# Kernel optimization log

Measured on AMD Instinct MI355X. Metric: run time of the kernel, lower is better.

## Reference

```python
import jax, jax.numpy as jnp
import numpy as np

N, E, D, H, L, R = 10000, 48000, 768, 4, 4, 3
NEG = -1e30


def setup_inputs() -> dict:
    key = jax.random.key(0)
    ks = jax.random.split(key, 16)
    s = 0.02
    return {
        'node_features': jax.random.normal(ks[0], (N, D), jnp.float32),
        'edge_index': jax.random.randint(ks[1], (2, E), 0, N, jnp.int64 if jax.config.jax_enable_x64 else jnp.int32),
        'edge_type': jax.random.randint(ks[2], (E,), 0, R, jnp.int64 if jax.config.jax_enable_x64 else jnp.int32),
        'rel_W': jax.random.normal(ks[3], (R, D, D), jnp.float32) * s,
        'rel_b': jnp.zeros((R, D), jnp.float32),
        'gat_W': jax.random.normal(ks[4], (L, D, H * D), jnp.float32) * s,
        'gat_att_src': jax.random.normal(ks[5], (L, H, D), jnp.float32) * s,
        'gat_att_dst': jax.random.normal(ks[6], (L, H, D), jnp.float32) * s,
        'gat_bias': jnp.zeros((L, D), jnp.float32),
        'proj_W1': jax.random.normal(ks[7], (D, 512), jnp.float32) * s,
        'proj_b1': jnp.zeros((512,), jnp.float32),
        'proj_W2': jax.random.normal(ks[8], (512, D), jnp.float32) * s,
        'proj_b2': jnp.zeros((D,), jnp.float32),
    }


def _gat_rel(g, a_src, a_dst, bias, src, dst, emask):
    # g: [N,H,D] transformed per-head node features; PyG GATConv with
    # add_self_loops=True, leaky_relu slope 0.2, concat=False (head mean).
    alpha_s = jnp.einsum('nhd,hd->nh', g, a_src)   # [N,H]
    alpha_d = jnp.einsum('nhd,hd->nh', g, a_dst)   # [N,H]
    e = jax.nn.leaky_relu(alpha_s[src] + alpha_d[dst], 0.2)  # [E,H]
    e = jnp.where(emask[:, None], e, NEG)          # mask other relations
    e_self = jax.nn.leaky_relu(alpha_s + alpha_d, 0.2)       # [N,H] self loops
    m = jax.ops.segment_max(e, dst, num_segments=N)
    m = jnp.maximum(m, e_self)                     # stable softmax max per dst
    p = jnp.where(emask[:, None], jnp.exp(e - m[dst]), 0.0)  # [E,H]
    p_self = jnp.exp(e_self - m)                   # [N,H]
    denom = jax.ops.segment_sum(p, dst, num_segments=N) + p_self
    msg = jax.ops.segment_sum(p[:, :, None] * g[src], dst, num_segments=N)
    msg = msg + p_self[:, :, None] * g             # [N,H,D]
    out = msg / denom[:, :, None]
    return out.mean(axis=1) + bias                 # concat=False -> head mean


def reference(node_features, edge_index, edge_type, rel_W, rel_b, gat_W,
              gat_att_src, gat_att_dst, gat_bias, proj_W1, proj_b1,
              proj_W2, proj_b2):
    src, dst = edge_index[0], edge_index[1]
    h = node_features
    for l in range(L):
        h_new = jnp.zeros_like(h)
        for r in range(R):
            emask = edge_type == r
            t = h @ rel_W[r] + rel_b[r]                    # relation transform
            g = (t @ gat_W[l]).reshape(N, H, D)            # [N,H,D]
            h_new = h_new + _gat_rel(g, gat_att_src[l], gat_att_dst[l],
                                     gat_bias[l], src, dst, emask)
        h = jax.nn.relu(h + h_new)                         # residual + relu
    positions = jax.nn.relu(h @ proj_W1 + proj_b1) @ proj_W2 + proj_b2
    return positions, h
```

## Files before the change

kernel.cpp:

```cpp
#include <hip/hip_runtime.h>
#include <stdint.h>

#define NN 10000
#define NE 48000
#define DIM 768
#define NH 4
#define NL 4
#define NR 3
#define HD 3072
#define NPAD 10240
#define NRD (NR*DIM)
#define SCN (NR*NN)
#define SCB ((SCN+255)/256)

typedef __attribute__((ext_vector_type(8))) short bf16x8;
typedef __attribute__((ext_vector_type(4))) float f32x4;

__device__ __forceinline__ unsigned short f2b(float f){
  union {float f; unsigned u;} v; v.f=f;
  unsigned r = v.u + 0x7FFFu + ((v.u>>16)&1u);
  return (unsigned short)(r>>16);
}
__device__ __forceinline__ float b2f(unsigned short b){
  union {unsigned u; float f;} v; v.u = ((unsigned)b)<<16; return v.f;
}

__device__ __forceinline__ void gl_lds16(const void* g, void* l){
  __builtin_amdgcn_global_load_lds(
    reinterpret_cast<const __attribute__((address_space(1))) uint32_t*>(reinterpret_cast<uintptr_t>(g)),
    reinterpret_cast<__attribute__((address_space(3))) uint32_t*>(reinterpret_cast<uintptr_t>(l)),
    16, 0, 0);
}

#define MPH(P) \
  { _Pragma("unroll") for (int ni=0; ni<NB; ni++) \
      _Pragma("unroll") for (int ks=0; ks<2; ks++) \
        acc[P][ni] = __builtin_amdgcn_mfma_f32_16x16x32_bf16( \
          a[P][ks], b[ni][ks], acc[P][ni],0,0,0); }

template<int MODE>
__global__ __launch_bounds__(512, 4)
void gemmU(const unsigned short* __restrict__ A, const unsigned short* __restrict__ Bt,
           void* __restrict__ C, unsigned short* __restrict__ C2,
           const float* __restrict__ RH, const float* __restrict__ bias, float bscale,
           int K, int Mvalid, int ldc)
{
  constexpr int NB     = 2;
  constexpr int ABYTES = 16384;
  constexpr int SLOT   = 32768;
  __shared__ char lds2[2*SLOT];

  const int tid = threadIdx.x;
  const int lane = tid & 63;
  const int wv = tid >> 6;
  const int wr = wv >> 2;
  const int wc = wv & 3;
  const int fr = lane & 15;
  const int fs = lane >> 4;

  int bx, by;
  {
    int fid = blockIdx.y * gridDim.x + blockIdx.x;
    if ((gridDim.y & 7) == 0){
      int xcd = fid & 7, slot = fid >> 3;
      bx = slot % gridDim.x;
      by = (slot / gridDim.x) * 8 + xcd;
    } else { bx = blockIdx.x; by = blockIdx.y; }
  }

  const unsigned short* Ag = A + (size_t)by * 128 * K;
  const unsigned short* Bg = Bt + (size_t)bx * 128 * K;
  const int T = K >> 6;

  f32x4 acc[4][NB];
  #pragma unroll
  for (int i=0;i<4;i++)
    #pragma unroll
    for (int j=0;j<NB;j++) acc[i][j] = (f32x4){0.f,0.f,0.f,0.f};

  auto stage = [&](int t2, int c){
    char* region = lds2 + (t2 & 1) * SLOT;
    const unsigned short* G = Ag;
    int off = c * 8192 + tid * 16;
    if (c >= 2){ G = Bg; off -= ABYTES; region += ABYTES; }
    int row = off >> 7;
    int srcslot = ((off >> 4) & 7) ^ (row & 7);
    gl_lds16((const char*)(G + (size_t)row * K + (size_t)t2 * 64) + (srcslot << 4),
             region + off);
  };

  #pragma unroll
  for (int c=0;c<4;c++) stage(0,c);
  __builtin_amdgcn_sched_barrier(0);
  stage(1,0); stage(1,1);
  __builtin_amdgcn_sched_barrier(0);

  for (int t=0; t<T; ++t){
    const char* As_ = lds2 + (t&1)*SLOT;
    const char* Bs_ = As_ + ABYTES;

    if (t < T-1) asm volatile("s_waitcnt vmcnt(2)" ::: "memory");
    else         asm volatile("s_waitcnt vmcnt(0)" ::: "memory");
    __builtin_amdgcn_s_barrier();

    bf16x8 a[4][2], b[NB][2];
    #pragma unroll
    for (int ni=0; ni<NB; ni++){
      const int row = wc*32 + ni*16 + fr;
      #pragma unroll
      for (int ks=0; ks<2; ks++){
        const int bo = row*128 + ((((ks<<2)+fs) ^ (row&7))<<4);
        b[ni][ks] = *(const bf16x8*)(Bs_ + bo);
      }
    }
    #pragma unroll
    for (int mi=0; mi<2; mi++){
      const int row = wr*64 + mi*16 + fr;
      #pragma unroll
      for (int ks=0; ks<2; ks++){
        const int bo = row*128 + ((((ks<<2)+fs) ^ (row&7))<<4);
        a[mi][ks] = *(const bf16x8*)(As_ + bo);
      }
    }
    if (t+1 < T) stage(t+1, 2);
    asm volatile("s_waitcnt lgkmcnt(0)" ::: "memory");
    __builtin_amdgcn_sched_barrier(0);
    __builtin_amdgcn_s_setprio(1); MPH(0); __builtin_amdgcn_s_setprio(0);
    __builtin_amdgcn_s_barrier();

    #pragma unroll
    for (int mi=2; mi<4; mi++){
      const int row = wr*64 + mi*16 + fr;
      #pragma unroll
      for (int ks=0; ks<2; ks++){
        const int bo = row*128 + ((((ks<<2)+fs) ^ (row&7))<<4);
        a[mi][ks] = *(const bf16x8*)(As_ + bo);
      }
    }
    if (t+1 < T) stage(t+1, 3);
    asm volatile("s_waitcnt lgkmcnt(0)" ::: "memory");
    __builtin_amdgcn_sched_barrier(0);
    __builtin_amdgcn_s_setprio(1); MPH(1); __builtin_amdgcn_s_setprio(0);
    __builtin_amdgcn_s_barrier();

    if (t+2 < T) stage(t+2, 0);
    __builtin_amdgcn_s_setprio(1); MPH(2); __builtin_amdgcn_s_setprio(0);
    __builtin_amdgcn_s_barrier();

    if (t+2 < T) stage(t+2, 1);
    __builtin_amdgcn_s_setprio(1); MPH(3); __builtin_amdgcn_s_setprio(0);
  }

  const int cr = (lane>>4)<<2, cc = lane&15;
  #pragma unroll
  for (int mi=0; mi<4; mi++){
    #pragma unroll
    for (int ni=0; ni<NB; ni++){
      const int col = bx*128 + wc*32 + ni*16 + cc;
      const float bv = bias ? bscale*bias[col] : 0.0f;
      #pragma unroll
      for (int j=0; j<4; j++){
        const int row = by*128 + wr*64 + mi*16 + cr + j;
        if (row < Mvalid){
          const size_t o = (size_t)row*ldc + col;
          float v = acc[mi][ni][j] + bv;
          if (MODE==2) v = v>0.f?v:0.f;
          if (MODE==0)      ((float*)C)[o] = v;
          else if (MODE==1 || MODE==2) ((unsigned short*)C)[o] = f2b(v);
          else {
            float w = RH[o] + v;
            w = w>0.f?w:0.f;
            ((float*)C)[o] = w; C2[o] = f2b(w);
          }
        }
      }
    }
  }
}

__global__ void k_init(const float* __restrict__ nf, float* __restrict__ h, unsigned short* __restrict__ hb){
  for (size_t i = (size_t)blockIdx.x*256+threadIdx.x; i < (size_t)NPAD*DIM; i += (size_t)gridDim.x*256){
    float v = (i < (size_t)NN*DIM) ? nf[i] : 0.0f;
    h[i]=v; hb[i]=f2b(v);
  }
}
__global__ void k_transpose(const float* __restrict__ in, unsigned short* __restrict__ out,
                            int rows, int cols, long in_bs, long out_bs){
  __shared__ float tile[32][33];
  int b = blockIdx.z;
  int r0 = blockIdx.y*32, c0 = blockIdx.x*32;
  int tx = threadIdx.x & 31, ty = threadIdx.x >> 5;
  const float* ip = in + (size_t)b*in_bs;
  unsigned short* op = out + (size_t)b*out_bs;
  #pragma unroll
  for (int i=ty;i<32;i+=8) tile[i][tx] = ip[(size_t)(r0+i)*cols + c0+tx];
  __syncthreads();
  #pragma unroll
  for (int i=ty;i<32;i+=8) op[(size_t)(c0+i)*rows + r0+tx] = f2b(tile[tx][i]);
}
__global__ void k_gatws(const float* __restrict__ gat_W, unsigned short* __restrict__ out){
  __shared__ float tile[32][33];
  int z = blockIdx.z; int l = z>>2, h = z&3;
  size_t base = (size_t)l*DIM*HD + (size_t)h*DIM;
  int r0 = blockIdx.y*32, c0 = blockIdx.x*32;
  int tx = threadIdx.x & 31, ty = threadIdx.x >> 5;
  #pragma unroll
  for (int i=ty;i<32;i+=8) tile[i][tx] = gat_W[base + (size_t)(r0+i)*HD + c0+tx];
  __syncthreads();
  #pragma unroll
  for (int i=ty;i<32;i+=8) out[base + (size_t)(c0+i)*HD + r0+tx] = f2b(0.25f*tile[tx][i]);
}

__global__ __launch_bounds__(256) void k_vsrc(const float* __restrict__ gat_W, const float* __restrict__ a_src,
                       const float* __restrict__ a_dst, float* __restrict__ vs, float* __restrict__ vd){
  int gw = blockIdx.x*4 + (threadIdx.x>>6);
  if (gw >= NL*DIM) return;
  int l = gw/DIM;
  int lane = threadIdx.x & 63;
  const float* grow = gat_W + (size_t)gw*HD;
  #pragma unroll
  for (int h=0;h<NH;h++){
    const float* asr = a_src + ((size_t)l*NH + h)*DIM;
    const float* adr = a_dst + ((size_t)l*NH + h)*DIM;
    float s=0.f,d=0.f;
    for (int dd=lane; dd<DIM; dd+=64){
      float gv = grow[h*DIM+dd];
      s += gv*asr[dd]; d += gv*adr[dd];
    }
    #pragma unroll
    for (int o=32;o>=1;o>>=1){ s += __shfl_xor(s,o,64); d += __shfl_xor(d,o,64); }
    if (lane==0){ vs[(size_t)gw*NH+h]=s; vd[(size_t)gw*NH+h]=d; }
  }
}
__global__ __launch_bounds__(256) void k_wa(const float* __restrict__ rel_W, const float* __restrict__ vs,
                     const float* __restrict__ vd, float* __restrict__ was, float* __restrict__ wad){
  int gw = blockIdx.x*4 + (threadIdx.x>>6);
  if (gw >= NL*NR*DIM) return;
  int lr = gw/DIM, k = gw%DIM;
  int l = lr/NR, r = lr%NR;
  int lane = threadIdx.x & 63;
  const float* wrow = rel_W + ((size_t)r*DIM + k)*DIM;
  float s0=0,s1=0,s2=0,s3=0,d0=0,d1=0,d2=0,d3=0;
  for (int q=lane; q<DIM; q+=64){
    float w = wrow[q];
    const float4 v1 = *(const float4*)(vs + ((size_t)l*DIM+q)*NH);
    const float4 v2 = *(const float4*)(vd + ((size_t)l*DIM+q)*NH);
    s0+=w*v1.x; s1+=w*v1.y; s2+=w*v1.z; s3+=w*v1.w;
    d0+=w*v2.x; d1+=w*v2.y; d2+=w*v2.z; d3+=w*v2.w;
  }
  #pragma unroll
  for (int o=32;o>=1;o>>=1){
    s0+=__shfl_xor(s0,o,64); s1+=__shfl_xor(s1,o,64); s2+=__shfl_xor(s2,o,64); s3+=__shfl_xor(s3,o,64);
    d0+=__shfl_xor(d0,o,64); d1+=__shfl_xor(d1,o,64); d2+=__shfl_xor(d2,o,64); d3+=__shfl_xor(d3,o,64);
  }
  if (lane==0){
    float4* ps = (float4*)(was + (size_t)gw*NH); *ps = make_float4(s0,s1,s2,s3);
    float4* pd = (float4*)(wad + (size_t)gw*NH); *pd = make_float4(d0,d1,d2,d3);
  }
}
__global__ void k_bsd(const float* __restrict__ rel_b, const float* __restrict__ vs, const float* __restrict__ vd,
                      float* __restrict__ bs, float* __restrict__ bd){
  int t = threadIdx.x; if (t >= NL*NR*NH) return;
  int l = t/(NR*NH), r = (t/NH)%NR, h = t%NH;
  float s=0.f,d=0.f;
  for (int q=0;q<DIM;q++){
    float b = rel_b[r*DIM+q];
    s += b*vs[((size_t)l*DIM+q)*NH+h];
    d += b*vd[((size_t)l*DIM+q)*NH+h];
  }
  bs[t]=s; bd[t]=d;
}

__global__ void k_count(const int* __restrict__ et, const int* __restrict__ ei, int* __restrict__ counts){
  int e = blockIdx.x*256+threadIdx.x; if (e>=NE) return;
  atomicAdd(&counts[et[e]*NN + ei[NE+e]], 1);
}
__global__ void k_scan1(const int* __restrict__ counts, int* __restrict__ excl, int* __restrict__ part){
  __shared__ int tmp[256];
  int b = blockIdx.x, t = threadIdx.x, idx = b*256+t;
  int v = (idx<SCN)? counts[idx] : 0;
  tmp[t]=v; __syncthreads();
  #pragma unroll
  for (int off=1; off<256; off<<=1){
    int x = (t>=off)? tmp[t-off] : 0;
    __syncthreads(); tmp[t]+=x; __syncthreads();
  }
  if (idx<SCN) excl[idx] = tmp[t]-v;
  if (t==255) part[b] = tmp[255];
}
__global__ void k_scan2(int* __restrict__ part){
  if (threadIdx.x==0){
    int c=0;
    for (int i=0;i<SCB;i++){ int v=part[i]; part[i]=c; c+=v; }
    part[SCB]=c;
  }
}
__global__ void k_scan3(int* __restrict__ rs, const int* __restrict__ part, int* __restrict__ cursor){
  int b = blockIdx.x, idx = b*256+threadIdx.x;
  if (idx<SCN){
    int e = rs[idx] + part[b];
    rs[idx]=e; cursor[idx]=e;
  }
  if (idx==0) rs[SCN] = part[SCB];
}
__global__ void k_fill(const int* __restrict__ et, const int* __restrict__ ei, int* __restrict__ cursor,
                       int* __restrict__ csrs, int* __restrict__ csre){
  int e = blockIdx.x*256+threadIdx.x; if (e>=NE) return;
  int pos = atomicAdd(&cursor[et[e]*NN + ei[NE+e]], 1);
  csrs[pos] = ei[e];
  csre[pos] = e;
}

__global__ __launch_bounds__(256) void k_alpha(const float* __restrict__ h,
    const float* __restrict__ WAS, const float* __restrict__ WAD,
    const float* __restrict__ BS, const float* __restrict__ BD,
    float* __restrict__ aS, float* __restrict__ aD,
    float* __restrict__ eself, float* __restrict__ mbuf, float* __restrict__ den, int l)
{
  int n = blockIdx.x*4 + (threadIdx.x>>6);
  if (n >= NN) return;
  int lane = threadIdx.x & 63;
  const float* hrow = h + (size_t)n*DIM;
  float hv[12];
  #pragma unroll
  for (int i=0;i<12;i++) hv[i] = hrow[lane + i*64];
  #pragma unroll
  for (int r=0;r<NR;r++){
    const float* was = WAS + ((size_t)(l*NR+r)*DIM)*NH;
    const float* wad = WAD + ((size_t)(l*NR+r)*DIM)*NH;
    float as[NH]={0,0,0,0}, ad[NH]={0,0,0,0};
    #pragma unroll
    for (int i=0;i<12;i++){
      int k = lane + i*64;
      const float4 wsv = *(const float4*)(was + (size_t)k*NH);
      const float4 wdv = *(const float4*)(wad + (size_t)k*NH);
      as[0]+=hv[i]*wsv.x; as[1]+=hv[i]*wsv.y; as[2]+=hv[i]*wsv.z; as[3]+=hv[i]*wsv.w;
      ad[0]+=hv[i]*wdv.x; ad[1]+=hv[i]*wdv.y; ad[2]+=hv[i]*wdv.z; ad[3]+=hv[i]*wdv.w;
    }
    #pragma unroll
    for (int o=32;o>=1;o>>=1){
      #pragma unroll
      for (int hh=0;hh<NH;hh++){
        as[hh] += __shfl_xor(as[hh], o, 64);
        ad[hh] += __shfl_xor(ad[hh], o, 64);
      }
    }
    if (lane==0){
      int rn = r*NN+n;
      #pragma unroll
      for (int hh=0;hh<NH;hh++){
        float A = as[hh]+BS[(l*NR+r)*NH+hh], B = ad[hh]+BD[(l*NR+r)*NH+hh];
        aS[rn*NH+hh]=A; aD[rn*NH+hh]=B;
        float es = A+B; es = es>0.f?es:0.2f*es;
        eself[rn*NH+hh]=es; mbuf[rn*NH+hh]=es; den[rn*NH+hh]=0.f;
      }
    }
  }
}
__device__ __forceinline__ void atomicMaxF(float* addr, float val){
  int* ia = (int*)addr;
  float curf = *((volatile float*)addr);
  while (val > curf){
    int old = atomicCAS(ia, __float_as_int(curf), __float_as_int(val));
    if (old == __float_as_int(curf)) break;
    curf = __int_as_float(old);
  }
}
__global__ void k_edge_max(const int* __restrict__ ei, const int* __restrict__ et,
                           const float* __restrict__ aS, const float* __restrict__ aD,
                           float* __restrict__ mbuf){
  int e = blockIdx.x*256+threadIdx.x; if (e>=NE) return;
  int r = et[e];
  int s = r*NN + ei[e], d = r*NN + ei[NE+e];
  #pragma unroll
  for (int hh=0;hh<NH;hh++){
    float x = aS[s*NH+hh] + aD[d*NH+hh]; x = x>0.f?x:0.2f*x;
    atomicMaxF(&mbuf[d*NH+hh], x);
  }
}
__global__ void k_edge_p(const int* __restrict__ ei, const int* __restrict__ et,
                         const float* __restrict__ aS, const float* __restrict__ aD,
                         const float* __restrict__ mbuf, float* __restrict__ den,
                         float* __restrict__ pbuf){
  int e = blockIdx.x*256+threadIdx.x; if (e>=NE) return;
  int r = et[e];
  int s = r*NN + ei[e], d = r*NN + ei[NE+e];
  #pragma unroll
  for (int hh=0;hh<NH;hh++){
    float x = aS[s*NH+hh] + aD[d*NH+hh]; x = x>0.f?x:0.2f*x;
    float p = __expf(x - mbuf[d*NH+hh]);
    pbuf[e*NH+hh]=p;
    atomicAdd(&den[d*NH+hh], p);
  }
}
__global__ __launch_bounds__(256) void k_aggz(const unsigned short* __restrict__ T3,
    const float* __restrict__ eself, const float* __restrict__ mbuf, const float* __restrict__ den,
    const float* __restrict__ pbuf, const int* __restrict__ row_start,
    const int* __restrict__ csrs, const int* __restrict__ csre,
    unsigned short* __restrict__ Z)
{
  int n = blockIdx.x, t = threadIdx.x;
  float z[3][NH];
  #pragma unroll
  for (int u=0;u<3;u++)
    #pragma unroll
    for (int hh=0;hh<NH;hh++) z[u][hh]=0.f;

  for (int r=0;r<NR;r++){
    int rn = r*NN+n;
    float ps[NH], inv[NH];
    #pragma unroll
    for (int hh=0;hh<NH;hh++){
      float p0 = __expf(eself[rn*NH+hh]-mbuf[rn*NH+hh]);
      ps[hh]=p0; inv[hh]=1.0f/(den[rn*NH+hh]+p0);
    }
    const unsigned short* tn = T3 + (size_t)n*NRD + r*DIM;
    float acc[3][NH];
    #pragma unroll
    for (int u=0;u<3;u++){
      float tv = b2f(tn[t+256*u]);
      #pragma unroll
      for (int hh=0;hh<NH;hh++) acc[u][hh] = ps[hh]*tv;
    }
    int beg = row_start[rn], end = row_start[rn+1];
    for (int p=beg;p<end;p++){
      int s = csrs[p]; int id = csre[p];
      float pe[NH];
      #pragma unroll
      for (int hh=0;hh<NH;hh++) pe[hh]=pbuf[id*NH+hh];
      const unsigned short* ts = T3 + (size_t)s*NRD + r*DIM;
      #pragma unroll
      for (int u=0;u<3;u++){
        float tv = b2f(ts[t+256*u]);
        #pragma unroll
        for (int hh=0;hh<NH;hh++) acc[u][hh] += pe[hh]*tv;
      }
    }
    #pragma unroll
    for (int u=0;u<3;u++)
      #pragma unroll
      for (int hh=0;hh<NH;hh++) z[u][hh] += inv[hh]*acc[u][hh];
  }
  #pragma unroll
  for (int u=0;u<3;u++)
    #pragma unroll
    for (int hh=0;hh<NH;hh++)
      Z[(size_t)n*HD + hh*DIM + t + 256*u] = f2b(z[u][hh]);
}

static constexpr size_t al(size_t x){ return (x + 255) & ~(size_t)255; }
static constexpr size_t OFF_H     = 0;
static constexpr size_t OFF_HB    = OFF_H    + al((size_t)NPAD*DIM*4);
static constexpr size_t OFF_T3    = OFF_HB   + al((size_t)NPAD*DIM*2);
static constexpr size_t OFF_Z     = OFF_T3   + al((size_t)NPAD*NRD*2);
static constexpr size_t OFF_GATWS = OFF_Z    + al((size_t)NPAD*HD*2);
static constexpr size_t OFF_RELWT = OFF_GATWS+ al((size_t)NL*DIM*HD*2);
static constexpr size_t OFF_W1T   = OFF_RELWT+ al((size_t)NR*DIM*DIM*2);
static constexpr size_t OFF_W2T   = OFF_W1T  + al((size_t)512*DIM*2);
static constexpr size_t OFF_ZP    = OFF_W2T  + al((size_t)DIM*512*2);
static constexpr size_t OFF_VS    = OFF_ZP   + al((size_t)NPAD*512*2);
static constexpr size_t OFF_VD    = OFF_VS   + al((size_t)NL*DIM*NH*4);
static constexpr size_t OFF_WAS   = OFF_VD   + al((size_t)NL*DIM*NH*4);
static constexpr size_t OFF_WAD   = OFF_WAS  + al((size_t)NL*NR*DIM*NH*4);
static constexpr size_t OFF_BS    = OFF_WAD  + al((size_t)NL*NR*DIM*NH*4);
static constexpr size_t OFF_BD    = OFF_BS   + al((size_t)NL*NR*NH*4);
static constexpr size_t OFF_AS    = OFF_BD   + al((size_t)NL*NR*NH*4);
static constexpr size_t OFF_AD    = OFF_AS   + al((size_t)SCN*NH*4);
static constexpr size_t OFF_ESELF = OFF_AD   + al((size_t)SCN*NH*4);
static constexpr size_t OFF_M     = OFF_ESELF+ al((size_t)SCN*NH*4);
static constexpr size_t OFF_DEN   = OFF_M    + al((size_t)SCN*NH*4);
static constexpr size_t OFF_PBUF  = OFF_DEN  + al((size_t)SCN*NH*4);
static constexpr size_t OFF_CNT   = OFF_PBUF + al((size_t)NE*NH*4);
static constexpr size_t OFF_RSTART= OFF_CNT  + al((size_t)SCN*4);
static constexpr size_t OFF_PART  = OFF_RSTART+al(((size_t)SCN+1)*4);
static constexpr size_t OFF_CUR   = OFF_PART + al(((size_t)SCB+1)*4);
static constexpr size_t OFF_CSRS  = OFF_CUR  + al((size_t)SCN*4);
static constexpr size_t OFF_CSRE  = OFF_CSRS + al((size_t)NE*4);

extern "C" void kernel_launch(void* const* d_in, const int* in_sizes, int n_in,
                              void* d_out, int out_size, void* d_ws, size_t ws_size,
                              hipStream_t stream) {
  const float* nf     = (const float*)d_in[0];
  const int*   ei     = (const int*)d_in[1];
  const int*   etype  = (const int*)d_in[2];
  const float* rel_W  = (const float*)d_in[3];
  const float* rel_b  = (const float*)d_in[4];
  const float* gat_W  = (const float*)d_in[5];
  const float* a_src  = (const float*)d_in[6];
  const float* a_dst  = (const float*)d_in[7];
  const float* gat_bias=(const float*)d_in[8];
  const float* pW1    = (const float*)d_in[9];
  const float* pb1    = (const float*)d_in[10];
  const float* pW2    = (const float*)d_in[11];
  const float* pb2    = (const float*)d_in[12];
  float* out = (float*)d_out;
  char* ws = (char*)d_ws;

  float*          H     = (float*)(ws+OFF_H);
  unsigned short* HB    = (unsigned short*)(ws+OFF_HB);
  unsigned short* T3    = (unsigned short*)(ws+OFF_T3);
  unsigned short* Z     = (unsigned short*)(ws+OFF_Z);
  unsigned short* GATWS = (unsigned short*)(ws+OFF_GATWS);
  unsigned short* RELWT = (unsigned short*)(ws+OFF_RELWT);
  unsigned short* W1T   = (unsigned short*)(ws+OFF_W1T);
  unsigned short* W2T   = (unsigned short*)(ws+OFF_W2T);
  unsigned short* ZP    = (unsigned short*)(ws+OFF_ZP);
  float* VS   = (float*)(ws+OFF_VS);
  float* VD   = (float*)(ws+OFF_VD);
  float* WAS  = (float*)(ws+OFF_WAS);
  float* WAD  = (float*)(ws+OFF_WAD);
  float* BS   = (float*)(ws+OFF_BS);
  float* BD   = (float*)(ws+OFF_BD);
  float* AS_  = (float*)(ws+OFF_AS);
  float* AD_  = (float*)(ws+OFF_AD);
  float* ESELF= (float*)(ws+OFF_ESELF);
  float* MBUF = (float*)(ws+OFF_M);
  float* DEN  = (float*)(ws+OFF_DEN);
  float* PBUF = (float*)(ws+OFF_PBUF);
  int* COUNTS = (int*)(ws+OFF_CNT);
  int* RSTART = (int*)(ws+OFF_RSTART);
  int* PART   = (int*)(ws+OFF_PART);
  int* CURSOR = (int*)(ws+OFF_CUR);
  int* CSRS   = (int*)(ws+OFF_CSRS);
  int* CSRE   = (int*)(ws+OFF_CSRE);

  k_init<<<2048,256,0,stream>>>(nf, H, HB);
  k_transpose<<<dim3(DIM/32, DIM/32, NR),256,0,stream>>>(rel_W, RELWT, DIM, DIM, (long)DIM*DIM, (long)DIM*DIM);
  k_gatws<<<dim3(DIM/32, DIM/32, NL*NH),256,0,stream>>>(gat_W, GATWS);
  k_transpose<<<dim3(512/32, DIM/32, 1),256,0,stream>>>(pW1, W1T, DIM, 512, 0, 0);
  k_transpose<<<dim3(DIM/32, 512/32, 1),256,0,stream>>>(pW2, W2T, 512, DIM, 0, 0);
  (void)hipMemsetAsync(COUNTS, 0, (size_t)SCN*4, stream);
  k_count<<<(NE+255)/256,256,0,stream>>>(etype, ei, COUNTS);
  k_scan1<<<SCB,256,0,stream>>>(COUNTS, RSTART, PART);
  k_scan2<<<1,64,0,stream>>>(PART);
  k_scan3<<<SCB,256,0,stream>>>(RSTART, PART, CURSOR);
  k_fill<<<(NE+255)/256,256,0,stream>>>(etype, ei, CURSOR, CSRS, CSRE);
  k_vsrc<<<NL*DIM/4,256,0,stream>>>(gat_W, a_src, a_dst, VS, VD);
  k_wa<<<NL*NR*DIM/4,256,0,stream>>>(rel_W, VS, VD, WAS, WAD);
  k_bsd<<<1,64,0,stream>>>(rel_b, VS, VD, BS, BD);

  for (int l=0; l<NL; l++){
    gemmU<1><<<dim3(NRD/128, NPAD/128),512,0,stream>>>(
        HB, RELWT, T3, nullptr, nullptr, rel_b, 1.0f, DIM, NN, NRD);
    k_alpha<<<(NN+3)/4,256,0,stream>>>(H, WAS, WAD, BS, BD, AS_, AD_, ESELF, MBUF, DEN, l);
    k_edge_max<<<(NE+255)/256,256,0,stream>>>(ei, etype, AS_, AD_, MBUF);
    k_edge_p<<<(NE+255)/256,256,0,stream>>>(ei, etype, AS_, AD_, MBUF, DEN, PBUF);
    k_aggz<<<NN,256,0,stream>>>(T3, ESELF, MBUF, DEN, PBUF, RSTART, CSRS, CSRE, Z);
    float* hw = (l==NL-1) ? (out + (size_t)NN*DIM) : H;
    gemmU<3><<<dim3(DIM/128, NPAD/128),512,0,stream>>>(
        Z, GATWS + (size_t)l*DIM*HD, hw, HB, H, gat_bias + (size_t)l*DIM, 3.0f, HD, NN, DIM);
  }

  gemmU<2><<<dim3(512/128, NPAD/128),512,0,stream>>>(
      HB, W1T, ZP, nullptr, nullptr, pb1, 1.0f, DIM, NN, 512);
  gemmU<0><<<dim3(DIM/128, NPAD/128),512,0,stream>>>(
      ZP, W2T, out, nullptr, nullptr, pb2, 1.0f, 512, NN, DIM);
}
```

Baseline: 966.4 us.

## Add 256x256-tile GEMM for relation transform and restructure gemmU LDS pipeline

Adds a new gemmT kernel with 256x256 output tiles, eight waves each computing a 128x64 sub-tile, and a double-buffered LDS pipeline that spreads prefetch stages across four MFMA quadrants. It replaces gemmU<1> for the per-layer relation transform GEMM (N x 768 -> N x 2304). The larger tile raises arithmetic intensity and cuts global loads per FLOP, at the cost of more registers and 128KB of LDS, which lowers occupancy and leaves fewer blocks (9x40) to fill the device. gemmU is also changed to load all A fragments up front, issue two prefetch stages together, and drop a wait and sched barrier in the middle phase.

```diff
diff --git a/kernel.cpp b/kernel.cpp
--- a/kernel.cpp
+++ b/kernel.cpp
@@ -105,6 +105,15 @@
 
     bf16x8 a[4][2], b[NB][2];
     #pragma unroll
+    for (int mi=0; mi<4; mi++){
+      const int row = wr*64 + mi*16 + fr;
+      #pragma unroll
+      for (int ks=0; ks<2; ks++){
+        const int bo = row*128 + ((((ks<<2)+fs) ^ (row&7))<<4);
+        a[mi][ks] = *(const bf16x8*)(As_ + bo);
+      }
+    }
+    #pragma unroll
     for (int ni=0; ni<NB; ni++){
       const int row = wc*32 + ni*16 + fr;
       #pragma unroll
@@ -113,41 +122,18 @@
         b[ni][ks] = *(const bf16x8*)(Bs_ + bo);
       }
     }
-    #pragma unroll
-    for (int mi=0; mi<2; mi++){
-      const int row = wr*64 + mi*16 + fr;
-      #pragma unroll
-      for (int ks=0; ks<2; ks++){
-        const int bo = row*128 + ((((ks<<2)+fs) ^ (row&7))<<4);
-        a[mi][ks] = *(const bf16x8*)(As_ + bo);
-      }
-    }
-    if (t+1 < T) stage(t+1, 2);
+    if (t+1 < T){ stage(t+1, 2); stage(t+1, 3); }
     asm volatile("s_waitcnt lgkmcnt(0)" ::: "memory");
-    __builtin_amdgcn_sched_barrier(0);
     __builtin_amdgcn_s_setprio(1); MPH(0); __builtin_amdgcn_s_setprio(0);
     __builtin_amdgcn_s_barrier();
 
-    #pragma unroll
-    for (int mi=2; mi<4; mi++){
-      const int row = wr*64 + mi*16 + fr;
-      #pragma unroll
-      for (int ks=0; ks<2; ks++){
-        const int bo = row*128 + ((((ks<<2)+fs) ^ (row&7))<<4);
-        a[mi][ks] = *(const bf16x8*)(As_ + bo);
-      }
-    }
-    if (t+1 < T) stage(t+1, 3);
-    asm volatile("s_waitcnt lgkmcnt(0)" ::: "memory");
-    __builtin_amdgcn_sched_barrier(0);
+    if (t+2 < T){ stage(t+2, 0); stage(t+2, 1); }
     __builtin_amdgcn_s_setprio(1); MPH(1); __builtin_amdgcn_s_setprio(0);
     __builtin_amdgcn_s_barrier();
 
-    if (t+2 < T) stage(t+2, 0);
     __builtin_amdgcn_s_setprio(1); MPH(2); __builtin_amdgcn_s_setprio(0);
     __builtin_amdgcn_s_barrier();
 
-    if (t+2 < T) stage(t+2, 1);
     __builtin_amdgcn_s_setprio(1); MPH(3); __builtin_amdgcn_s_setprio(0);
   }
 
@@ -172,6 +158,132 @@
             w = w>0.f?w:0.f;
             ((float*)C)[o] = w; C2[o] = f2b(w);
           }
+        }
+      }
+    }
+  }
+}
+
+#define QUAD(MH,NH_) \
+  { _Pragma("unroll") for (int mi=0; mi<4; mi++) \
+      _Pragma("unroll") for (int ni=0; ni<2; ni++) \
+        _Pragma("unroll") for (int ks=0; ks<2; ks++) \
+          acc[(MH)*4+mi][(NH_)*2+ni] = __builtin_amdgcn_mfma_f32_16x16x32_bf16( \
+            a[(MH)*4+mi][ks], b[(NH_)*2+ni][ks], acc[(MH)*4+mi][(NH_)*2+ni],0,0,0); }
+
+__global__ __launch_bounds__(512, 2)
+void gemmT(const unsigned short* __restrict__ A, const unsigned short* __restrict__ Bt,
+           unsigned short* __restrict__ C, const float* __restrict__ bias,
+           int K, int Mvalid, int ldc)
+{
+  constexpr int ABYTES = 32768;
+  constexpr int CPT    = 8;
+  constexpr int SLOT   = ABYTES + 32768;
+  __shared__ char lds2[2*SLOT];
+
+  const int tid = threadIdx.x;
+  const int lane = tid & 63;
+  const int wv = tid >> 6;
+  const int wr = wv >> 2;
+  const int wc = wv & 3;
+  const int fr = lane & 15;
+  const int fs = lane >> 4;
+
+  int nb  = gridDim.x * gridDim.y;
+  int fid = blockIdx.y * gridDim.x + blockIdx.x;
+  if ((nb & 7) == 0){
+    int per = nb >> 3;
+    fid = (fid & 7) * per + (fid >> 3);
+  }
+  const int bx = fid % gridDim.x;
+  const int by = fid / gridDim.x;
+
+  const unsigned short* Ag = A + (size_t)by * 256 * K;
+  const unsigned short* Bg = Bt + (size_t)bx * 256 * K;
+  const int T = K >> 6;
+
+  f32x4 acc[8][4];
+  #pragma unroll
+  for (int i=0;i<8;i++)
+    #pragma unroll
+    for (int j=0;j<4;j++) acc[i][j] = (f32x4){0.f,0.f,0.f,0.f};
+
+  auto stage = [&](int t2, int c){
+    char* region = lds2 + (t2 & 1) * SLOT;
+    const unsigned short* G = Ag;
+    int off = c * 8192 + tid * 16;
+    if (c >= 4){ G = Bg; off -= ABYTES; region += ABYTES; }
+    int row = off >> 7;
+    int srcslot = ((off >> 4) & 7) ^ (row & 7);
+    gl_lds16((const char*)(G + (size_t)row * K + (size_t)t2 * 64) + (srcslot << 4),
+             region + off);
+  };
+
+  #pragma unroll
+  for (int c=0;c<CPT;c++) stage(0,c);
+  __builtin_amdgcn_sched_barrier(0);
+  #pragma unroll
+  for (int c=0;c<CPT-2;c++) stage(1,c);
+  __builtin_amdgcn_sched_barrier(0);
+
+  for (int t=0; t<T; ++t){
+    const char* As_ = lds2 + (t&1)*SLOT;
+    const char* Bs_ = As_ + ABYTES;
+
+    if (t < T-1) asm volatile("s_waitcnt vmcnt(6)" ::: "memory");
+    else         asm volatile("s_waitcnt vmcnt(0)" ::: "memory");
+    __builtin_amdgcn_s_barrier();
+
+    bf16x8 a[8][2], b[4][2];
+    #pragma unroll
+    for (int mi=0; mi<8; mi++){
+      const int row = wr*128 + mi*16 + fr;
+      #pragma unroll
+      for (int ks=0; ks<2; ks++){
+        const int bo = row*128 + ((((ks<<2)+fs) ^ (row&7))<<4);
+        a[mi][ks] = *(const bf16x8*)(As_ + bo);
+      }
+    }
+    #pragma unroll
+    for (int ni=0; ni<4; ni++){
+      const int row = wc*64 + ni*16 + fr;
+      #pragma unroll
+      for (int ks=0; ks<2; ks++){
+        const int bo = row*128 + ((((ks<<2)+fs) ^ (row&7))<<4);
+        b[ni][ks] = *(const bf16x8*)(Bs_ + bo);
+      }
+    }
+    if (t+1 < T){ stage(t+1, CPT-2); stage(t+1, CPT-1); }
+    asm volatile("s_waitcnt lgkmcnt(0)" ::: "memory");
+    __builtin_amdgcn_s_setprio(1); QUAD(0,0); __builtin_amdgcn_s_setprio(0);
+    __builtin_amdgcn_s_barrier();
+
+    const bool pf = (t+2 < T);
+    if (pf){ stage(t+2,0); stage(t+2,1); }
+    __builtin_amdgcn_s_setprio(1); QUAD(0,1); __builtin_amdgcn_s_setprio(0);
+    __builtin_amdgcn_s_barrier();
+
+    if (pf){ stage(t+2,2); stage(t+2,3); }
+    __builtin_amdgcn_s_setprio(1); QUAD(1,0); __builtin_amdgcn_s_setprio(0);
+    __builtin_amdgcn_s_barrier();
+
+    if (pf){ stage(t+2,4); stage(t+2,5); }
+    __builtin_amdgcn_s_setprio(1); QUAD(1,1); __builtin_amdgcn_s_setprio(0);
+  }
+
+  const int cr = (lane>>4)<<2, cc = lane&15;
+  #pragma unroll
+  for (int mi=0; mi<8; mi++){
+    #pragma unroll
+    for (int ni=0; ni<4; ni++){
+      const int col = bx*256 + wc*64 + ni*16 + cc;
+      const float bv = bias ? bias[col] : 0.0f;
+      #pragma unroll
+      for (int j=0; j<4; j++){
+        const int row = by*256 + wr*128 + mi*16 + cr + j;
+        if (row < Mvalid){
+          float v = acc[mi][ni][j] + bv;
+          C[(size_t)row*ldc + col] = f2b(v);
         }
       }
     }
@@ -540,8 +652,8 @@
   k_bsd<<<1,64,0,stream>>>(rel_b, VS, VD, BS, BD);
 
   for (int l=0; l<NL; l++){
-    gemmU<1><<<dim3(NRD/128, NPAD/128),512,0,stream>>>(
-        HB, RELWT, T3, nullptr, nullptr, rel_b, 1.0f, DIM, NN, NRD);
+    gemmT<<<dim3(NRD/256, NPAD/256),512,0,stream>>>(
+        HB, RELWT, T3, rel_b, DIM, NN, NRD);
     k_alpha<<<(NN+3)/4,256,0,stream>>>(H, WAS, WAD, BS, BD, AS_, AD_, ESELF, MBUF, DEN, l);
     k_edge_max<<<(NE+255)/256,256,0,stream>>>(ei, etype, AS_, AD_, MBUF);
     k_edge_p<<<(NE+255)/256,256,0,stream>>>(ei, etype, AS_, AD_, MBUF, DEN, PBUF);
```

After: 1.082 ms. 11.9% more time.
